# Performance work log

Hardware: AMD Instinct MI355X
Metric: run time of the kernel (lower is better)

The kernel has to match this reference:

```python
import jax, jax.numpy as jnp
import numpy as np

TOP_K = 2

def _mlp(x, w_gate_up, b_gate_up, w_down):
    # x: [T,H]; w_gate_up: [2I,H]; b_gate_up: [2I]; w_down: [H,I]
    gu = x @ w_gate_up.T + b_gate_up
    i = w_gate_up.shape[0] // 2
    h = jax.nn.silu(gu[..., :i]) * gu[..., i:]  # SiluAndMul
    return h @ w_down.T

def setup_inputs() -> dict:
    key = jax.random.key(0)
    ks = jax.random.split(key, 8)
    T, H, I, E = 8192, 1024, 512, 16
    s = 0.02  # weight init scale
    return {
        "hidden_states": jax.random.normal(ks[0], (T, H), jnp.float32),
        "gate_w": jax.random.normal(ks[1], (E, H), jnp.float32) * s,
        "w_gate_up": jax.random.normal(ks[2], (E, 2 * I, H), jnp.float32) * s,
        "b_gate_up": jax.random.normal(ks[3], (E, 2 * I), jnp.float32) * s,
        "w_down": jax.random.normal(ks[4], (E, H, I), jnp.float32) * s,
        "ws_gate_up": jax.random.normal(ks[5], (2 * I, H), jnp.float32) * s,
        "bs_gate_up": jax.random.normal(ks[6], (2 * I,), jnp.float32) * s,
        "ws_down": jax.random.normal(ks[7], (H, I), jnp.float32) * s,
    }

def reference(hidden_states, gate_w, w_gate_up, b_gate_up, w_down,
              ws_gate_up, bs_gate_up, ws_down):
    x = hidden_states  # [T,H]
    E = gate_w.shape[0]

    # shared expert
    shared_out = _mlp(x, ws_gate_up, bs_gate_up, ws_down)  # [T,H]

    # router: softmax in float32, then top-k and renormalize (norm_topk_prob)
    router_logits = x @ gate_w.T  # [T,E]
    probs = jax.nn.softmax(router_logits.astype(jnp.float32), axis=-1)
    rw, sel = jax.lax.top_k(probs, TOP_K)  # [T,K]
    rw = rw / jnp.sum(rw, axis=-1, keepdims=True)

    # per-token per-expert weight [T,E] (0 for unselected experts)
    ew = jnp.sum(jax.nn.one_hot(sel, E, dtype=rw.dtype) * rw[..., None], axis=1)

    # dense all-experts MLP (faithful to the naive masked loop, vectorized)
    gu = jnp.einsum('th,eih->eti', x, w_gate_up) + b_gate_up[:, None, :]  # [E,T,2I]
    I = gu.shape[-1] // 2
    act = jax.nn.silu(gu[..., :I]) * gu[..., I:]  # [E,T,I]
    # scaling by routing weight commutes with the linear down_proj
    wact = act * ew.T[:, :, None].astype(act.dtype)  # [E,T,I]
    final = jnp.einsum('eti,ehi->th', wact, w_down)  # [T,H]

    return final + shared_out
```

## Files before the change

kernel.cpp:

```cpp
#include <hip/hip_runtime.h>
#include <hip/hip_bf16.h>
#include <cstdint>
#include <cstddef>

typedef _Float16 f16;
typedef _Float16 f16x4 __attribute__((ext_vector_type(4)));
typedef _Float16 f16x8 __attribute__((ext_vector_type(8)));
typedef float f32x4 __attribute__((ext_vector_type(4)));

#define GPTR(p) ((const __attribute__((address_space(1))) void*)(p))
#define LPTR(p) ((__attribute__((address_space(3))) void*)(p))

#define T_TOK 8192
#define H_DIM 1024
#define I_DIM 512
#define N_EXP 16
#define N_ALL 17
#define TOPK 2
#define NSLOT (T_TOK * TOPK)
#define NSLOT_ALL (NSLOT + T_TOK)

#define MAX_TILES 208
#define XCD_TILES (MAX_TILES / 8)
#define NXCD 8

#define PREP_BLOCKS 34338
__global__ void prep_kernel(const float* __restrict__ x, const float* __restrict__ gw,
                            const float* __restrict__ wgu, const float* __restrict__ wsgu,
                            const float* __restrict__ wd, const float* __restrict__ wsd,
                            const float* __restrict__ bgu, const float* __restrict__ bsgu,
                            f16* __restrict__ x_h, f16* __restrict__ x_l,
                            f16* __restrict__ gw_h, f16* __restrict__ gw_l,
                            f16* __restrict__ wguA, f16* __restrict__ wdA,
                            float* __restrict__ biasA, int* __restrict__ counts) {
    const int bid = blockIdx.x, tid = threadIdx.x;
    if (bid < 8192) {
        int i = bid * 256 + tid;
        float4 v = ((const float4*)x)[i];
        float vv[4] = { v.x, v.y, v.z, v.w };
        f16x4 h, l;
#pragma unroll
        for (int r = 0; r < 4; r++) { h[r] = (f16)vv[r]; l[r] = (f16)(vv[r] - (float)h[r]); }
        *(f16x4*)(x_h + (size_t)i * 4) = h;
        *(f16x4*)(x_l + (size_t)i * 4) = l;
    } else if (bid < 8208) {
        int i = (bid - 8192) * 256 + tid;
        float4 v = ((const float4*)gw)[i];
        float vv[4] = { v.x, v.y, v.z, v.w };
        f16x4 h, l;
#pragma unroll
        for (int r = 0; r < 4; r++) { h[r] = (f16)vv[r]; l[r] = (f16)(vv[r] - (float)h[r]); }
        *(f16x4*)(gw_h + (size_t)i * 4) = h;
        *(f16x4*)(gw_l + (size_t)i * 4) = l;
    } else if (bid < 24592) {
        int i = (bid - 8208) * 256 + tid;
        float4 v = ((const float4*)wgu)[i];
        f16x4 o = { (f16)v.x, (f16)v.y, (f16)v.z, (f16)v.w };
        *(f16x4*)(wguA + (size_t)i * 4) = o;
    } else if (bid < 25616) {
        int i = (bid - 24592) * 256 + tid;
        float4 v = ((const float4*)wsgu)[i];
        f16x4 o = { (f16)v.x, (f16)v.y, (f16)v.z, (f16)v.w };
        *(f16x4*)(wguA + (size_t)16 * 1024 * 1024 + (size_t)i * 4) = o;
    } else if (bid < 33808) {
        int i = (bid - 25616) * 256 + tid;
        float4 v = ((const float4*)wd)[i];
        f16x4 o = { (f16)v.x, (f16)v.y, (f16)v.z, (f16)v.w };
        *(f16x4*)(wdA + (size_t)i * 4) = o;
    } else if (bid < 34320) {
        int i = (bid - 33808) * 256 + tid;
        float4 v = ((const float4*)wsd)[i];
        f16x4 o = { (f16)v.x, (f16)v.y, (f16)v.z, (f16)v.w };
        *(f16x4*)(wdA + (size_t)16 * 1024 * 512 + (size_t)i * 4) = o;
    } else if (bid < 34336) {
        int i = (bid - 34320) * 256 + tid;
        ((float4*)biasA)[i] = ((const float4*)bgu)[i];
    } else if (bid == 34336) {
        ((float4*)(biasA + 16384))[tid] = ((const float4*)bsgu)[tid];
    } else {
        if (tid < 16) counts[tid] = 0;
    }
}

__global__ __launch_bounds__(256) void logits_kernel(
    const f16* __restrict__ Xh, const f16* __restrict__ Xl,
    const f16* __restrict__ Gh, const f16* __restrict__ Gl,
    float* __restrict__ L) {
    const int wave = threadIdx.x >> 6, lane = threadIdx.x & 63;
    const int m0 = blockIdx.x * 64 + wave * 16;
    const int qm = lane & 15, quad = lane >> 4;
    const size_t arow = (size_t)(m0 + qm) * H_DIM + quad * 8;
    const size_t brow = (size_t)qm * H_DIM + quad * 8;
    f32x4 acc = (f32x4){0.f, 0.f, 0.f, 0.f};
    const f16* ap;
    const f16* bp;
    ap = Xh + arow; bp = Gh + brow;
#pragma unroll 8
    for (int k0 = 0; k0 < H_DIM; k0 += 32) {
        acc = __builtin_amdgcn_mfma_f32_16x16x32_f16(*(const f16x8*)ap, *(const f16x8*)bp, acc, 0, 0, 0);
        ap += 32; bp += 32;
    }
    ap = Xh + arow; bp = Gl + brow;
#pragma unroll 8
    for (int k0 = 0; k0 < H_DIM; k0 += 32) {
        acc = __builtin_amdgcn_mfma_f32_16x16x32_f16(*(const f16x8*)ap, *(const f16x8*)bp, acc, 0, 0, 0);
        ap += 32; bp += 32;
    }
    ap = Xl + arow; bp = Gh + brow;
#pragma unroll 8
    for (int k0 = 0; k0 < H_DIM; k0 += 32) {
        acc = __builtin_amdgcn_mfma_f32_16x16x32_f16(*(const f16x8*)ap, *(const f16x8*)bp, acc, 0, 0, 0);
        ap += 32; bp += 32;
    }
#pragma unroll
    for (int r = 0; r < 4; r++)
        L[(size_t)(m0 + quad * 4 + r) * N_EXP + qm] = acc[r];
}

__global__ void topk_kernel(const float* __restrict__ L, int* __restrict__ sel,
                            float* __restrict__ rw, int* __restrict__ counts) {
    __shared__ int lc[N_EXP];
    const int tid = threadIdx.x;
    if (tid < N_EXP) lc[tid] = 0;
    __syncthreads();
    const int t = blockIdx.x * 256 + tid;
    float lg[16];
    const float4* lp = (const float4*)(L + (size_t)t * N_EXP);
#pragma unroll
    for (int q = 0; q < 4; q++) {
        float4 v = lp[q];
        lg[q * 4 + 0] = v.x; lg[q * 4 + 1] = v.y; lg[q * 4 + 2] = v.z; lg[q * 4 + 3] = v.w;
    }
    float best = -1e30f, sec = -1e30f; int bi = 0, si = 0;
#pragma unroll
    for (int j = 0; j < 16; j++) {
        float lj = lg[j];
        if (lj > best) { sec = best; si = bi; best = lj; bi = j; }
        else if (lj > sec) { sec = lj; si = j; }
    }
    float w1 = 1.f / (1.f + __expf(sec - best));
    sel[t * 2] = bi; sel[t * 2 + 1] = si;
    rw[t * 2] = w1;  rw[t * 2 + 1] = 1.f - w1;
    atomicAdd(&lc[bi], 1);
    atomicAdd(&lc[si], 1);
    __syncthreads();
    if (tid < N_EXP) atomicAdd(&counts[tid], lc[tid]);
}

__global__ void prefix_kernel(const int* __restrict__ counts, int* __restrict__ offsets,
                              int* __restrict__ cursors, int* __restrict__ tiles) {
    if (threadIdx.x == 0) {
        int s = 0;
        for (int e = 0; e < N_EXP; e++) { offsets[e] = s; cursors[e] = s; s += counts[e]; }
        offsets[N_EXP] = s;
        offsets[N_EXP + 1] = s + T_TOK;
        int nt = 0;
        for (int m0 = 0; m0 < T_TOK; m0 += 128) tiles[nt++] = (16 << 20) | m0;
        for (int e = 0; e < N_EXP; e++) {
            int M = counts[e];
            for (int m0 = 0; m0 < M; m0 += 128) tiles[nt++] = (e << 20) | m0;
        }
        for (; nt < MAX_TILES; nt++) tiles[nt] = -1;
    }
}

__global__ void scatter_kernel(const int* __restrict__ sel, const float* __restrict__ rw,
                               int* __restrict__ cursors, int* __restrict__ btok,
                               float* __restrict__ bw, int* __restrict__ pos) {
    int t = blockIdx.x * blockDim.x + threadIdx.x;
    if (t >= T_TOK) return;
#pragma unroll
    for (int k = 0; k < TOPK; k++) {
        int e = sel[t * 2 + k];
        int p = atomicAdd(&cursors[e], 1);
        btok[p] = t;
        bw[p] = rw[t * 2 + k];
        pos[t * 2 + k] = p;
    }
    btok[NSLOT + t] = t;
    bw[NSLOT + t] = 1.f;
}

__device__ __forceinline__ void xcd_tile_map(int g, int& ti, int& n0i) {
    const int x = g & 7;
    const int q = g >> 3;
    ti  = x * XCD_TILES + (q >> 3);
    n0i = q & 7;
}

__global__ __launch_bounds__(256, 4) void gemm_gateup_act(
    const f16* __restrict__ X,
    const f16* __restrict__ W,
    const float* __restrict__ bias,
    const float* __restrict__ bw,
    f16* __restrict__ ACT,
    const int* __restrict__ offsets,
    const int* __restrict__ btok,
    const int* __restrict__ tiles) {
    constexpr int K = H_DIM;
    int ti, n0i;
    xcd_tile_map(blockIdx.x, ti, n0i);
    const int td = tiles[ti];
    if (td < 0) return;
    const int e  = td >> 20;
    const int m0 = td & 0xFFFFF;
    const int n0 = n0i * 64;
    const int base = offsets[e];
    const int M = offsets[e + 1] - base;

    const f16* Wb   = W + (size_t)e * 1024 * K;
    const float* bb = bias + (size_t)e * 1024;

    __shared__ f16 As[2][128 * 32];
    __shared__ f16 Bg[2][64 * 32];
    __shared__ f16 Bu[2][64 * 32];

    const int tid  = threadIdx.x;
    const int wave = tid >> 6;
    const int lane = tid & 63;
    const int srow = lane >> 2;
    const int scol = (lane & 3) * 8;

    int ar0 = m0 + wave * 32 + srow;
    int ar1 = ar0 + 16;
    int r0 = min(ar0, M - 1), r1 = min(ar1, M - 1);
    const f16* ap0 = X + (size_t)btok[base + r0] * K + scol;
    const f16* ap1 = X + (size_t)btok[base + r1] * K + scol;
    const int brow = n0 + wave * 16 + srow;
    const f16* bg0 = Wb + (size_t)brow * K + scol;
    const f16* bu0 = bg0 + (size_t)512 * K;
    f16* la0 = &As[0][(wave * 32) * 32];
    f16* la1 = la0 + 16 * 32;
    f16* lg0 = &Bg[0][(wave * 16) * 32];
    f16* lu0 = &Bu[0][(wave * 16) * 32];
    constexpr int AST = 128 * 32;
    constexpr int BST = 64 * 32;

    const int wm = (wave >> 1) * 64;
    const int wn = (wave & 1) * 32;
    const int qm = lane & 15;
    const int quad = lane >> 4;

    f32x4 accg[4][2], accu[4][2];
#pragma unroll
    for (int i = 0; i < 4; i++)
#pragma unroll
        for (int j = 0; j < 2; j++) {
            accg[i][j] = (f32x4){0.f, 0.f, 0.f, 0.f};
            accu[i][j] = (f32x4){0.f, 0.f, 0.f, 0.f};
        }

#define GU_STAGE(b) do { \
    __builtin_amdgcn_global_load_lds(GPTR(ap0), LPTR(la0 + (b) * AST), 16, 0, 0); \
    __builtin_amdgcn_global_load_lds(GPTR(ap1), LPTR(la1 + (b) * AST), 16, 0, 0); \
    __builtin_amdgcn_global_load_lds(GPTR(bg0), LPTR(lg0 + (b) * BST), 16, 0, 0); \
    __builtin_amdgcn_global_load_lds(GPTR(bu0), LPTR(lu0 + (b) * BST), 16, 0, 0); \
    ap0 += 32; ap1 += 32; bg0 += 32; bu0 += 32; } while (0)

#define GU_COMPUTE(b) do { \
    f16x8 af[4], gf[2], uf[2]; \
    _Pragma("unroll") \
    for (int i = 0; i < 4; i++) af[i] = *(const f16x8*)&As[b][(wm + i * 16 + qm) * 32 + quad * 8]; \
    _Pragma("unroll") \
    for (int j = 0; j < 2; j++) { \
        gf[j] = *(const f16x8*)&Bg[b][(wn + j * 16 + qm) * 32 + quad * 8]; \
        uf[j] = *(const f16x8*)&Bu[b][(wn + j * 16 + qm) * 32 + quad * 8]; \
    } \
    _Pragma("unroll") \
    for (int i = 0; i < 4; i++) \
        _Pragma("unroll") \
        for (int j = 0; j < 2; j++) { \
            accg[i][j] = __builtin_amdgcn_mfma_f32_16x16x32_f16(af[i], gf[j], accg[i][j], 0, 0, 0); \
            accu[i][j] = __builtin_amdgcn_mfma_f32_16x16x32_f16(af[i], uf[j], accu[i][j], 0, 0, 0); \
        } } while (0)

    GU_STAGE(0);
    __syncthreads();
    for (int t = 0; t < K / 32; t += 2) {
        GU_STAGE(1);
        GU_COMPUTE(0);
        __syncthreads();
        if (t + 2 < K / 32) GU_STAGE(0);
        GU_COMPUTE(1);
        __syncthreads();
    }

#pragma unroll
    for (int i = 0; i < 4; i++) {
#pragma unroll
        for (int j = 0; j < 2; j++) {
            const int colg = n0 + wn + j * 16 + qm;
            const float bvg = bb[colg];
            const float bvu = bb[colg + 512];
#pragma unroll
            for (int r = 0; r < 4; r++) {
                const int lr = wm + i * 16 + quad * 4 + r;
                const int m = m0 + lr;
                if (m < M) {
                    float g = accg[i][j][r] + bvg;
                    float u = accu[i][j][r] + bvu;
                    float sl = g / (1.f + __expf(-g));
                    ACT[(size_t)(base + m) * 512 + colg] = (f16)(sl * u * bw[base + m]);
                }
            }
        }
    }
}

__global__ __launch_bounds__(256, 4) void gemm_down(
    const f16* __restrict__ ACT,
    const f16* __restrict__ W,
    f16* __restrict__ DOWN,
    const int* __restrict__ offsets,
    const int* __restrict__ tiles) {
    constexpr int K = I_DIM;
    int ti, n0i;
    xcd_tile_map(blockIdx.x, ti, n0i);
    const int td = tiles[ti];
    if (td < 0) return;
    const int e  = td >> 20;
    const int m0 = td & 0xFFFFF;
    const int n0 = n0i * 128;
    const int base = offsets[e];
    const int M = offsets[e + 1] - base;

    const f16* Wb = W + (size_t)e * 1024 * K;

    __shared__ f16 As[2][128 * 32];
    __shared__ f16 Bs[2][128 * 32];

    const int tid  = threadIdx.x;
    const int wave = tid >> 6;
    const int lane = tid & 63;
    const int srow = lane >> 2;
    const int scol = (lane & 3) * 8;

    int ar0 = m0 + wave * 32 + srow;
    int ar1 = ar0 + 16;
    int r0 = min(ar0, M - 1), r1 = min(ar1, M - 1);
    const f16* ap0 = ACT + (size_t)(base + r0) * K + scol;
    const f16* ap1 = ACT + (size_t)(base + r1) * K + scol;
    const f16* bp0 = Wb + (size_t)(n0 + wave * 32 + srow) * K + scol;
    const f16* bp1 = bp0 + (size_t)16 * K;
    f16* la0 = &As[0][(wave * 32) * 32];  f16* la1 = la0 + 16 * 32;
    f16* lb0 = &Bs[0][(wave * 32) * 32];  f16* lb1 = lb0 + 16 * 32;
    constexpr int DST = 128 * 32;

    const int wm = (wave >> 1) * 64;
    const int wn = (wave & 1) * 64;
    const int qm = lane & 15;
    const int quad = lane >> 4;

    f32x4 acc[4][4];
#pragma unroll
    for (int i = 0; i < 4; i++)
#pragma unroll
        for (int j = 0; j < 4; j++) acc[i][j] = (f32x4){0.f, 0.f, 0.f, 0.f};

#define DN_STAGE(b) do { \
    __builtin_amdgcn_global_load_lds(GPTR(ap0), LPTR(la0 + (b) * DST), 16, 0, 0); \
    __builtin_amdgcn_global_load_lds(GPTR(ap1), LPTR(la1 + (b) * DST), 16, 0, 0); \
    __builtin_amdgcn_global_load_lds(GPTR(bp0), LPTR(lb0 + (b) * DST), 16, 0, 0); \
    __builtin_amdgcn_global_load_lds(GPTR(bp1), LPTR(lb1 + (b) * DST), 16, 0, 0); \
    ap0 += 32; ap1 += 32; bp0 += 32; bp1 += 32; } while (0)

#define DN_COMPUTE(b) do { \
    f16x8 af[4], bfr[4]; \
    _Pragma("unroll") \
    for (int i = 0; i < 4; i++) af[i]  = *(const f16x8*)&As[b][(wm + i * 16 + qm) * 32 + quad * 8]; \
    _Pragma("unroll") \
    for (int j = 0; j < 4; j++) bfr[j] = *(const f16x8*)&Bs[b][(wn + j * 16 + qm) * 32 + quad * 8]; \
    _Pragma("unroll") \
    for (int i = 0; i < 4; i++) \
        _Pragma("unroll") \
        for (int j = 0; j < 4; j++) \
            acc[i][j] = __builtin_amdgcn_mfma_f32_16x16x32_f16(af[i], bfr[j], acc[i][j], 0, 0, 0); \
    } while (0)

    DN_STAGE(0);
    __syncthreads();
    for (int t = 0; t < K / 32; t += 2) {
        DN_STAGE(1);
        DN_COMPUTE(0);
        __syncthreads();
        if (t + 2 < K / 32) DN_STAGE(0);
        DN_COMPUTE(1);
        __syncthreads();
    }

#pragma unroll
    for (int i = 0; i < 4; i++) {
#pragma unroll
        for (int j = 0; j < 4; j++) {
            const int col = n0 + wn + j * 16 + qm;
#pragma unroll
            for (int r = 0; r < 4; r++) {
                const int lr = wm + i * 16 + quad * 4 + r;
                const int m = m0 + lr;
                if (m < M) DOWN[(size_t)(base + m) * 1024 + col] = (f16)acc[i][j][r];
            }
        }
    }
}

__global__ void combine_kernel(const f16* __restrict__ DOWN, const int* __restrict__ pos,
                               float* __restrict__ OUT) {
    int idx = blockIdx.x * blockDim.x + threadIdx.x;
    int t = idx >> 8;
    int c = (idx & 255) * 4;
    int p1 = pos[t * 2], p2 = pos[t * 2 + 1];
    f16x4 a = *(const f16x4*)(DOWN + (size_t)(NSLOT + t) * 1024 + c);
    f16x4 b = *(const f16x4*)(DOWN + (size_t)p1 * 1024 + c);
    f16x4 d = *(const f16x4*)(DOWN + (size_t)p2 * 1024 + c);
    float4 o;
    o.x = (float)a[0] + (float)b[0] + (float)d[0];
    o.y = (float)a[1] + (float)b[1] + (float)d[1];
    o.z = (float)a[2] + (float)b[2] + (float)d[2];
    o.w = (float)a[3] + (float)b[3] + (float)d[3];
    *(float4*)(OUT + (size_t)t * 1024 + c) = o;
}

extern "C" void kernel_launch(void* const* d_in, const int* in_sizes, int n_in,
                              void* d_out, int out_size, void* d_ws, size_t ws_size,
                              hipStream_t stream) {
    const float* x    = (const float*)d_in[0];
    const float* gw   = (const float*)d_in[1];
    const float* wgu  = (const float*)d_in[2];
    const float* bgu  = (const float*)d_in[3];
    const float* wd   = (const float*)d_in[4];
    const float* wsgu = (const float*)d_in[5];
    const float* bsgu = (const float*)d_in[6];
    const float* wsd  = (const float*)d_in[7];
    float* out = (float*)d_out;

    char* ws = (char*)d_ws;
    size_t off = 0;
    auto take = [&](size_t b) { char* p = ws + off; off = (off + b + 255) & ~(size_t)255; return p; };
    f16* x_h    = (f16*)take((size_t)T_TOK * H_DIM * 2);
    f16* x_l    = (f16*)take((size_t)T_TOK * H_DIM * 2);
    f16* gw_h   = (f16*)take((size_t)N_EXP * H_DIM * 2);
    f16* gw_l   = (f16*)take((size_t)N_EXP * H_DIM * 2);
    f16* wguA   = (f16*)take((size_t)N_ALL * 1024 * H_DIM * 2);
    f16* wdA    = (f16*)take((size_t)N_ALL * 1024 * I_DIM * 2);
    float* biasA = (float*)take((size_t)N_ALL * 1024 * 4);
    f16* act    = (f16*)take((size_t)NSLOT_ALL * I_DIM * 2);
    f16* down   = (f16*)take((size_t)NSLOT_ALL * 1024 * 2);
    float* logits = (float*)take((size_t)T_TOK * N_EXP * 4);
    int*   sel    = (int*)take((size_t)NSLOT * 4);
    float* rw     = (float*)take((size_t)NSLOT * 4);
    int*   btok   = (int*)take((size_t)NSLOT_ALL * 4);
    float* bw     = (float*)take((size_t)NSLOT_ALL * 4);
    int*   pos    = (int*)take((size_t)NSLOT * 4);
    int*   counts = (int*)take(64);
    int*   offs   = (int*)take(128);
    int*   curs   = (int*)take(64);
    int*   tiles  = (int*)take(MAX_TILES * 4);

    prep_kernel<<<PREP_BLOCKS, 256, 0, stream>>>(x, gw, wgu, wsgu, wd, wsd, bgu, bsgu,
                                                 x_h, x_l, gw_h, gw_l, wguA, wdA, biasA, counts);

    logits_kernel<<<T_TOK / 64, 256, 0, stream>>>(x_h, x_l, gw_h, gw_l, logits);
    topk_kernel<<<T_TOK / 256, 256, 0, stream>>>(logits, sel, rw, counts);
    prefix_kernel<<<1, 64, 0, stream>>>(counts, offs, curs, tiles);
    scatter_kernel<<<T_TOK / 256, 256, 0, stream>>>(sel, rw, curs, btok, bw, pos);

    gemm_gateup_act<<<dim3(MAX_TILES * 8, 1, 1), 256, 0, stream>>>(x_h, wguA, biasA, bw, act, offs, btok, tiles);

    gemm_down<<<dim3(MAX_TILES * 8, 1, 1), 256, 0, stream>>>(act, wdA, down, offs, tiles);

    combine_kernel<<<T_TOK * 1024 / 4 / 256, 256, 0, stream>>>(down, pos, out);
}
```

Before: 406.4 us.

## Use triple-buffered LDS pipeline with partial vmcnt waits in expert GEMMs

```diff
diff --git a/kernel.cpp b/kernel.cpp
--- a/kernel.cpp
+++ b/kernel.cpp
@@ -188,6 +188,19 @@
     n0i = q & 7;
 }
 
+#define PIPE_WAIT4() do { \
+    __builtin_amdgcn_sched_barrier(0); \
+    asm volatile("s_waitcnt vmcnt(4)" ::: "memory"); \
+    __builtin_amdgcn_sched_barrier(0); \
+    __builtin_amdgcn_s_barrier(); \
+    __builtin_amdgcn_sched_barrier(0); } while (0)
+#define PIPE_WAIT0() do { \
+    __builtin_amdgcn_sched_barrier(0); \
+    asm volatile("s_waitcnt vmcnt(0)" ::: "memory"); \
+    __builtin_amdgcn_sched_barrier(0); \
+    __builtin_amdgcn_s_barrier(); \
+    __builtin_amdgcn_sched_barrier(0); } while (0)
+
 __global__ __launch_bounds__(256, 4) void gemm_gateup_act(
     const f16* __restrict__ X,
     const f16* __restrict__ W,
@@ -198,6 +211,7 @@
     const int* __restrict__ btok,
     const int* __restrict__ tiles) {
     constexpr int K = H_DIM;
+    constexpr int NT = K / 32;
     int ti, n0i;
     xcd_tile_map(blockIdx.x, ti, n0i);
     const int td = tiles[ti];
@@ -211,9 +225,9 @@
     const f16* Wb   = W + (size_t)e * 1024 * K;
     const float* bb = bias + (size_t)e * 1024;
 
-    __shared__ f16 As[2][128 * 32];
-    __shared__ f16 Bg[2][64 * 32];
-    __shared__ f16 Bu[2][64 * 32];
+    __shared__ f16 As[3][128 * 32];
+    __shared__ f16 Bg[3][64 * 32];
+    __shared__ f16 Bu[3][64 * 32];
 
     const int tid  = threadIdx.x;
     const int wave = tid >> 6;
@@ -275,15 +289,17 @@
         } } while (0)
 
     GU_STAGE(0);
-    __syncthreads();
-    for (int t = 0; t < K / 32; t += 2) {
-        GU_STAGE(1);
-        GU_COMPUTE(0);
-        __syncthreads();
-        if (t + 2 < K / 32) GU_STAGE(0);
-        GU_COMPUTE(1);
-        __syncthreads();
-    }
+    GU_STAGE(1);
+    int bc = 0, bs = 2;
+    for (int t = 0; t < NT - 2; t++) {
+        PIPE_WAIT4();
+        GU_STAGE(bs); bs = (bs == 2) ? 0 : bs + 1;
+        GU_COMPUTE(bc); bc = (bc == 2) ? 0 : bc + 1;
+    }
+    PIPE_WAIT4();
+    GU_COMPUTE(bc); bc = (bc == 2) ? 0 : bc + 1;
+    PIPE_WAIT0();
+    GU_COMPUTE(bc);
 
 #pragma unroll
     for (int i = 0; i < 4; i++) {
@@ -314,6 +330,7 @@
     const int* __restrict__ offsets,
     const int* __restrict__ tiles) {
     constexpr int K = I_DIM;
+    constexpr int NT = K / 32;
     int ti, n0i;
     xcd_tile_map(blockIdx.x, ti, n0i);
     const int td = tiles[ti];
@@ -326,8 +343,8 @@
 
     const f16* Wb = W + (size_t)e * 1024 * K;
 
-    __shared__ f16 As[2][128 * 32];
-    __shared__ f16 Bs[2][128 * 32];
+    __shared__ f16 As[3][128 * 32];
+    __shared__ f16 Bs[3][128 * 32];
 
     const int tid  = threadIdx.x;
     const int wave = tid >> 6;
@@ -378,15 +395,17 @@
     } while (0)
 
     DN_STAGE(0);
-    __syncthreads();
-    for (int t = 0; t < K / 32; t += 2) {
-        DN_STAGE(1);
-        DN_COMPUTE(0);
-        __syncthreads();
-        if (t + 2 < K / 32) DN_STAGE(0);
-        DN_COMPUTE(1);
-        __syncthreads();
-    }
+    DN_STAGE(1);
+    int bc = 0, bs = 2;
+    for (int t = 0; t < NT - 2; t++) {
+        PIPE_WAIT4();
+        DN_STAGE(bs); bs = (bs == 2) ? 0 : bs + 1;
+        DN_COMPUTE(bc); bc = (bc == 2) ? 0 : bc + 1;
+    }
+    PIPE_WAIT4();
+    DN_COMPUTE(bc); bc = (bc == 2) ? 0 : bc + 1;
+    PIPE_WAIT0();
+    DN_COMPUTE(bc);
 
 #pragma unroll
     for (int i = 0; i < 4; i++) {
```

After: 418.9 us. 1.03x slower.

## Fuse combine into down GEMM via atomics, swizzle LDS, relax GEMM barriers

Applied to the files above, without the earlier changes.

```diff
diff --git a/kernel.cpp b/kernel.cpp
--- a/kernel.cpp
+++ b/kernel.cpp
@@ -22,9 +22,8 @@
 
 #define MAX_TILES 208
 #define XCD_TILES (MAX_TILES / 8)
-#define NXCD 8
-
-#define PREP_BLOCKS 34338
+
+#define PREP_BLOCKS 42530
 __global__ void prep_kernel(const float* __restrict__ x, const float* __restrict__ gw,
                             const float* __restrict__ wgu, const float* __restrict__ wsgu,
                             const float* __restrict__ wd, const float* __restrict__ wsd,
@@ -32,7 +31,8 @@
                             f16* __restrict__ x_h, f16* __restrict__ x_l,
                             f16* __restrict__ gw_h, f16* __restrict__ gw_l,
                             f16* __restrict__ wguA, f16* __restrict__ wdA,
-                            float* __restrict__ biasA, int* __restrict__ counts) {
+                            float* __restrict__ biasA, int* __restrict__ counts,
+                            float* __restrict__ out0) {
     const int bid = blockIdx.x, tid = threadIdx.x;
     if (bid < 8192) {
         int i = bid * 256 + tid;
@@ -77,8 +77,11 @@
         ((float4*)biasA)[i] = ((const float4*)bgu)[i];
     } else if (bid == 34336) {
         ((float4*)(biasA + 16384))[tid] = ((const float4*)bsgu)[tid];
+    } else if (bid == 34337) {
+        if (tid < 16) counts[tid] = 0;
     } else {
-        if (tid < 16) counts[tid] = 0;
+        size_t i = (size_t)(bid - 34338) * 256 + tid;
+        ((float4*)out0)[i] = (float4){0.f, 0.f, 0.f, 0.f};
     }
 }
 
@@ -166,7 +169,7 @@
 
 __global__ void scatter_kernel(const int* __restrict__ sel, const float* __restrict__ rw,
                                int* __restrict__ cursors, int* __restrict__ btok,
-                               float* __restrict__ bw, int* __restrict__ pos) {
+                               float* __restrict__ bw) {
     int t = blockIdx.x * blockDim.x + threadIdx.x;
     if (t >= T_TOK) return;
 #pragma unroll
@@ -175,7 +178,6 @@
         int p = atomicAdd(&cursors[e], 1);
         btok[p] = t;
         bw[p] = rw[t * 2 + k];
-        pos[t * 2 + k] = p;
     }
     btok[NSLOT + t] = t;
     bw[NSLOT + t] = 1.f;
@@ -187,6 +189,13 @@
     ti  = x * XCD_TILES + (q >> 3);
     n0i = q & 7;
 }
+
+#define WAITV4_BAR() do { \
+    asm volatile("s_waitcnt vmcnt(4)" ::: "memory"); \
+    __builtin_amdgcn_s_barrier(); } while (0)
+#define WAITV0_BAR() do { \
+    asm volatile("s_waitcnt vmcnt(0)" ::: "memory"); \
+    __builtin_amdgcn_s_barrier(); } while (0)
 
 __global__ __launch_bounds__(256, 4) void gemm_gateup_act(
     const f16* __restrict__ X,
@@ -198,6 +207,7 @@
     const int* __restrict__ btok,
     const int* __restrict__ tiles) {
     constexpr int K = H_DIM;
+    constexpr int NT = K / 32;
     int ti, n0i;
     xcd_tile_map(blockIdx.x, ti, n0i);
     const int td = tiles[ti];
@@ -219,15 +229,15 @@
     const int wave = tid >> 6;
     const int lane = tid & 63;
     const int srow = lane >> 2;
-    const int scol = (lane & 3) * 8;
+    const int csw  = ((lane & 3) ^ ((srow >> 1) & 3)) * 8;
 
     int ar0 = m0 + wave * 32 + srow;
     int ar1 = ar0 + 16;
     int r0 = min(ar0, M - 1), r1 = min(ar1, M - 1);
-    const f16* ap0 = X + (size_t)btok[base + r0] * K + scol;
-    const f16* ap1 = X + (size_t)btok[base + r1] * K + scol;
+    const f16* ap0 = X + (size_t)btok[base + r0] * K + csw;
+    const f16* ap1 = X + (size_t)btok[base + r1] * K + csw;
     const int brow = n0 + wave * 16 + srow;
-    const f16* bg0 = Wb + (size_t)brow * K + scol;
+    const f16* bg0 = Wb + (size_t)brow * K + csw;
     const f16* bu0 = bg0 + (size_t)512 * K;
     f16* la0 = &As[0][(wave * 32) * 32];
     f16* la1 = la0 + 16 * 32;
@@ -240,6 +250,7 @@
     const int wn = (wave & 1) * 32;
     const int qm = lane & 15;
     const int quad = lane >> 4;
+    const int qsw = (quad ^ ((qm >> 1) & 3)) * 8;
 
     f32x4 accg[4][2], accu[4][2];
 #pragma unroll
@@ -260,11 +271,11 @@
 #define GU_COMPUTE(b) do { \
     f16x8 af[4], gf[2], uf[2]; \
     _Pragma("unroll") \
-    for (int i = 0; i < 4; i++) af[i] = *(const f16x8*)&As[b][(wm + i * 16 + qm) * 32 + quad * 8]; \
+    for (int i = 0; i < 4; i++) af[i] = *(const f16x8*)&As[b][(wm + i * 16 + qm) * 32 + qsw]; \
     _Pragma("unroll") \
     for (int j = 0; j < 2; j++) { \
-        gf[j] = *(const f16x8*)&Bg[b][(wn + j * 16 + qm) * 32 + quad * 8]; \
-        uf[j] = *(const f16x8*)&Bu[b][(wn + j * 16 + qm) * 32 + quad * 8]; \
+        gf[j] = *(const f16x8*)&Bg[b][(wn + j * 16 + qm) * 32 + qsw]; \
+        uf[j] = *(const f16x8*)&Bu[b][(wn + j * 16 + qm) * 32 + qsw]; \
     } \
     _Pragma("unroll") \
     for (int i = 0; i < 4; i++) \
@@ -275,14 +286,19 @@
         } } while (0)
 
     GU_STAGE(0);
-    __syncthreads();
-    for (int t = 0; t < K / 32; t += 2) {
+    for (int t = 0; t < NT; t += 2) {
+        __builtin_amdgcn_s_barrier();
         GU_STAGE(1);
+        WAITV4_BAR();
         GU_COMPUTE(0);
-        __syncthreads();
-        if (t + 2 < K / 32) GU_STAGE(0);
+        __builtin_amdgcn_s_barrier();
+        if (t + 2 < NT) {
+            GU_STAGE(0);
+            WAITV4_BAR();
+        } else {
+            WAITV0_BAR();
+        }
         GU_COMPUTE(1);
-        __syncthreads();
     }
 
 #pragma unroll
@@ -310,10 +326,12 @@
 __global__ __launch_bounds__(256, 4) void gemm_down(
     const f16* __restrict__ ACT,
     const f16* __restrict__ W,
-    f16* __restrict__ DOWN,
+    float* __restrict__ OUT,
     const int* __restrict__ offsets,
+    const int* __restrict__ btok,
     const int* __restrict__ tiles) {
     constexpr int K = I_DIM;
+    constexpr int NT = K / 32;
     int ti, n0i;
     xcd_tile_map(blockIdx.x, ti, n0i);
     const int td = tiles[ti];
@@ -333,14 +351,14 @@
     const int wave = tid >> 6;
     const int lane = tid & 63;
     const int srow = lane >> 2;
-    const int scol = (lane & 3) * 8;
+    const int csw  = ((lane & 3) ^ ((srow >> 1) & 3)) * 8;
 
     int ar0 = m0 + wave * 32 + srow;
     int ar1 = ar0 + 16;
     int r0 = min(ar0, M - 1), r1 = min(ar1, M - 1);
-    const f16* ap0 = ACT + (size_t)(base + r0) * K + scol;
-    const f16* ap1 = ACT + (size_t)(base + r1) * K + scol;
-    const f16* bp0 = Wb + (size_t)(n0 + wave * 32 + srow) * K + scol;
+    const f16* ap0 = ACT + (size_t)(base + r0) * K + csw;
+    const f16* ap1 = ACT + (size_t)(base + r1) * K + csw;
+    const f16* bp0 = Wb + (size_t)(n0 + wave * 32 + srow) * K + csw;
     const f16* bp1 = bp0 + (size_t)16 * K;
     f16* la0 = &As[0][(wave * 32) * 32];  f16* la1 = la0 + 16 * 32;
     f16* lb0 = &Bs[0][(wave * 32) * 32];  f16* lb1 = lb0 + 16 * 32;
@@ -350,6 +368,7 @@
     const int wn = (wave & 1) * 64;
     const int qm = lane & 15;
     const int quad = lane >> 4;
+    const int qsw = (quad ^ ((qm >> 1) & 3)) * 8;
 
     f32x4 acc[4][4];
 #pragma unroll
@@ -367,9 +386,9 @@
 #define DN_COMPUTE(b) do { \
     f16x8 af[4], bfr[4]; \
     _Pragma("unroll") \
-    for (int i = 0; i < 4; i++) af[i]  = *(const f16x8*)&As[b][(wm + i * 16 + qm) * 32 + quad * 8]; \
-    _Pragma("unroll") \
-    for (int j = 0; j < 4; j++) bfr[j] = *(const f16x8*)&Bs[b][(wn + j * 16 + qm) * 32 + quad * 8]; \
+    for (int i = 0; i < 4; i++) af[i]  = *(const f16x8*)&As[b][(wm + i * 16 + qm) * 32 + qsw]; \
+    _Pragma("unroll") \
+    for (int j = 0; j < 4; j++) bfr[j] = *(const f16x8*)&Bs[b][(wn + j * 16 + qm) * 32 + qsw]; \
     _Pragma("unroll") \
     for (int i = 0; i < 4; i++) \
         _Pragma("unroll") \
@@ -378,46 +397,36 @@
     } while (0)
 
     DN_STAGE(0);
-    __syncthreads();
-    for (int t = 0; t < K / 32; t += 2) {
+    for (int t = 0; t < NT; t += 2) {
+        __builtin_amdgcn_s_barrier();
         DN_STAGE(1);
+        WAITV4_BAR();
         DN_COMPUTE(0);
-        __syncthreads();
-        if (t + 2 < K / 32) DN_STAGE(0);
+        __builtin_amdgcn_s_barrier();
+        if (t + 2 < NT) {
+            DN_STAGE(0);
+            WAITV4_BAR();
+        } else {
+            WAITV0_BAR();
+        }
         DN_COMPUTE(1);
-        __syncthreads();
     }
 
 #pragma unroll
     for (int i = 0; i < 4; i++) {
 #pragma unroll
-        for (int j = 0; j < 4; j++) {
-            const int col = n0 + wn + j * 16 + qm;
-#pragma unroll
-            for (int r = 0; r < 4; r++) {
-                const int lr = wm + i * 16 + quad * 4 + r;
-                const int m = m0 + lr;
-                if (m < M) DOWN[(size_t)(base + m) * 1024 + col] = (f16)acc[i][j][r];
+        for (int r = 0; r < 4; r++) {
+            const int lr = wm + i * 16 + quad * 4 + r;
+            const int m = m0 + lr;
+            if (m < M) {
+                const int tok = btok[base + m];
+                float* orow = OUT + (size_t)tok * 1024 + n0 + wn + qm;
+#pragma unroll
+                for (int j = 0; j < 4; j++)
+                    atomicAdd(orow + j * 16, acc[i][j][r]);
             }
         }
     }
-}
-
-__global__ void combine_kernel(const f16* __restrict__ DOWN, const int* __restrict__ pos,
-                               float* __restrict__ OUT) {
-    int idx = blockIdx.x * blockDim.x + threadIdx.x;
-    int t = idx >> 8;
-    int c = (idx & 255) * 4;
-    int p1 = pos[t * 2], p2 = pos[t * 2 + 1];
-    f16x4 a = *(const f16x4*)(DOWN + (size_t)(NSLOT + t) * 1024 + c);
-    f16x4 b = *(const f16x4*)(DOWN + (size_t)p1 * 1024 + c);
-    f16x4 d = *(const f16x4*)(DOWN + (size_t)p2 * 1024 + c);
-    float4 o;
-    o.x = (float)a[0] + (float)b[0] + (float)d[0];
-    o.y = (float)a[1] + (float)b[1] + (float)d[1];
-    o.z = (float)a[2] + (float)b[2] + (float)d[2];
-    o.w = (float)a[3] + (float)b[3] + (float)d[3];
-    *(float4*)(OUT + (size_t)t * 1024 + c) = o;
 }
 
 extern "C" void kernel_launch(void* const* d_in, const int* in_sizes, int n_in,
@@ -444,29 +453,26 @@
     f16* wdA    = (f16*)take((size_t)N_ALL * 1024 * I_DIM * 2);
     float* biasA = (float*)take((size_t)N_ALL * 1024 * 4);
     f16* act    = (f16*)take((size_t)NSLOT_ALL * I_DIM * 2);
-    f16* down   = (f16*)take((size_t)NSLOT_ALL * 1024 * 2);
     float* logits = (float*)take((size_t)T_TOK * N_EXP * 4);
     int*   sel    = (int*)take((size_t)NSLOT * 4);
     float* rw     = (float*)take((size_t)NSLOT * 4);
     int*   btok   = (int*)take((size_t)NSLOT_ALL * 4);
     float* bw     = (float*)take((size_t)NSLOT_ALL * 4);
-    int*   pos    = (int*)take((size_t)NSLOT * 4);
     int*   counts = (int*)take(64);
     int*   offs   = (int*)take(128);
     int*   curs   = (int*)take(64);
     int*   tiles  = (int*)take(MAX_TILES * 4);
 
     prep_kernel<<<PREP_BLOCKS, 256, 0, stream>>>(x, gw, wgu, wsgu, wd, wsd, bgu, bsgu,
-                                                 x_h, x_l, gw_h, gw_l, wguA, wdA, biasA, counts);
+                                                 x_h, x_l, gw_h, gw_l, wguA, wdA, biasA,
+                                                 counts, out);
 
     logits_kernel<<<T_TOK / 64, 256, 0, stream>>>(x_h, x_l, gw_h, gw_l, logits);
     topk_kernel<<<T_TOK / 256, 256, 0, stream>>>(logits, sel, rw, counts);
     prefix_kernel<<<1, 64, 0, stream>>>(counts, offs, curs, tiles);
-    scatter_kernel<<<T_TOK / 256, 256, 0, stream>>>(sel, rw, curs, btok, bw, pos);
+    scatter_kernel<<<T_TOK / 256, 256, 0, stream>>>(sel, rw, curs, btok, bw);
 
     gemm_gateup_act<<<dim3(MAX_TILES * 8, 1, 1), 256, 0, stream>>>(x_h, wguA, biasA, bw, act, offs, btok, tiles);
 
-    gemm_down<<<dim3(MAX_TILES * 8, 1, 1), 256, 0, stream>>>(act, wdA, down, offs, tiles);
-
-    combine_kernel<<<T_TOK * 1024 / 4 / 256, 256, 0, stream>>>(down, pos, out);
-}
+    gemm_down<<<dim3(MAX_TILES * 8, 1, 1), 256, 0, stream>>>(act, wdA, out, offs, btok, tiles);
+}
```

Measured after the change: 427.0 us. 1.05x slower.
